# Optimization experiments

Measured on AMD Instinct MI355X. Metric: run time of the kernel, lower is better.

## Reference

```python
import jax, jax.numpy as jnp
import numpy as np

N, D, B, R, EF, K = 500000, 128, 512, 32, 64, 10
INF = 1e30  # sentinel distance for dead/duplicate slots


def setup_inputs() -> dict:
    key = jax.random.key(0)
    k1, k2, k3, k4 = jax.random.split(key, 4)
    return {
        "query": jax.random.normal(k1, (B, D), jnp.float32),
        "storage": jax.random.normal(k2, (N, D), jnp.float32),
        "indices": jax.random.randint(k3, (N, R), 0, N, dtype=jnp.int32),
        "entry": jax.random.randint(k4, (B, EF), 0, N, dtype=jnp.int32),
        "k": K,
        "ef_search": EF,
    }


def _merge(ids, dists, expanded, ef):
    # Dedup by node id (prefer the already-expanded copy so nodes are never
    # re-expanded), then keep the ef best candidates by distance.
    key = ids * 2 + (1 - expanded.astype(ids.dtype))  # expanded copy sorts first
    order = jnp.argsort(key)  # stable sort
    ids, dists, expanded = ids[order], dists[order], expanded[order]
    dup = jnp.concatenate([jnp.zeros((1,), bool), ids[1:] == ids[:-1]])
    dists = jnp.where(dup, INF, dists)       # kill duplicate slots
    expanded = jnp.where(dup, True, expanded)  # dead slots never selected
    order = jnp.argsort(dists)
    return ids[order][:ef], dists[order][:ef], expanded[order][:ef]


def _search_one(q, ep, storage, indices, ef):
    # Beam (priority-list) best-first NSW traversal for a single query,
    # ef steps of expand-best-unexpanded, batched-friendly formulation.
    d0 = jnp.sum((storage[ep] - q) ** 2, axis=-1)  # squared-L2 distances
    state = _merge(ep, d0, jnp.zeros(ep.shape, bool), ef)

    def step(carry, _):
        ids, dists, expanded = carry
        sel = jnp.argmin(jnp.where(expanded, INF, dists))  # best open node
        expanded = expanded.at[sel].set(True)
        nbrs = indices[ids[sel]]                           # [R] neighbor ids
        nd = jnp.sum((storage[nbrs] - q) ** 2, axis=-1)    # [R] distances
        carry = _merge(
            jnp.concatenate([ids, nbrs]),
            jnp.concatenate([dists, nd]),
            jnp.concatenate([expanded, jnp.zeros((R,), bool)]),
            ef,
        )
        return carry, None

    (ids, dists, _), _ = jax.lax.scan(step, state, None, length=ef)
    return ids, dists


def reference(query, storage, indices, entry, k, ef_search):
    ids, dists = jax.vmap(_search_one, in_axes=(0, 0, None, None, None))(
        query, entry, storage, indices, ef_search
    )
    return ids[:, :k], dists[:, :k]
```

## Files before the change

kernel.cpp:

```cpp
#include <hip/hip_runtime.h>
#include <stdint.h>

#define DIM 128
#define RNB 32
#define EFS 64
#define KTOP 10
#define INFD 1e30f

typedef unsigned long long u64;

__device__ __forceinline__ u64 shflx64(u64 v, int m) {
    return (u64)__shfl_xor((long long)v, m, 64);
}
__device__ __forceinline__ u64 dsperm64(int dst_byte, u64 v) {
    int lo = __builtin_amdgcn_ds_permute(dst_byte, (int)(unsigned)(v & 0xffffffffu));
    int hi = __builtin_amdgcn_ds_permute(dst_byte, (int)(unsigned)(v >> 32));
    return ((u64)(unsigned)hi << 32) | (unsigned)lo;
}
__device__ __forceinline__ u64 readlane64(u64 v, int l) {
    unsigned lo = (unsigned)__builtin_amdgcn_readlane((int)(unsigned)(v & 0xffffffffu), l);
    unsigned hi = (unsigned)__builtin_amdgcn_readlane((int)(unsigned)(v >> 32), l);
    return ((u64)hi << 32) | lo;
}
template <int CTRL>
__device__ __forceinline__ float dpp_add(float x) {
    int y = __builtin_amdgcn_mov_dpp(__float_as_int(x), CTRL, 0xF, 0xF, true);
    return x + __int_as_float(y);
}

__device__ __forceinline__ void bitonic128(u64 &e0, u64 &e1, int lane) {
    #pragma unroll
    for (int k = 2; k <= 128; k <<= 1) {
        #pragma unroll
        for (int j = k >> 1; j >= 1; j >>= 1) {
            if (j == 64) {
                u64 lo = e0 < e1 ? e0 : e1;
                u64 hi = e0 < e1 ? e1 : e0;
                e0 = lo; e1 = hi;
            } else {
                u64 o0 = shflx64(e0, j);
                u64 o1 = shflx64(e1, j);
                int i0 = lane, i1 = lane + 64;
                bool keepmin0 = ((i0 & k) == 0) == ((i0 & j) == 0);
                bool keepmin1 = ((i1 & k) == 0) == ((i1 & j) == 0);
                e0 = keepmin0 ? (e0 < o0 ? e0 : o0) : (e0 > o0 ? e0 : o0);
                e1 = keepmin1 ? (e1 < o1 ? e1 : o1) : (e1 > o1 ? e1 : o1);
            }
        }
    }
}

__device__ __forceinline__ void merge_slow(int n, int lane,
                                           int* ids_s, float* dst_s, int* exp_s,
                                           int* ids2, float* dst2, int* exp2) {
    __syncthreads();
    {
        int i1 = lane + 64;
        u64 e0 = ((u64)(uint32_t)(ids_s[lane] * 2 + (exp_s[lane] ? 0 : 1)) << 32) | (uint32_t)lane;
        u64 e1 = ~0ULL;
        if (i1 < n)
            e1 = ((u64)(uint32_t)(ids_s[i1] * 2 + (exp_s[i1] ? 0 : 1)) << 32) | (uint32_t)i1;
        bitonic128(e0, e1, lane);

        int id0 = -1, id1 = -1; float d0 = INFD, d1 = INFD; int x0 = 1, x1 = 1;
        { int p = (int)(e0 & 0xffffffffu); id0 = ids_s[p]; d0 = dst_s[p]; x0 = exp_s[p]; }
        if (e1 != ~0ULL) { int p = (int)(e1 & 0xffffffffu); id1 = ids_s[p]; d1 = dst_s[p]; x1 = exp_s[p]; }

        int prev0 = __shfl_up(id0, 1);
        int top0  = __shfl(id0, 63);
        int prev1 = __shfl_up(id1, 1);
        bool dup0 = (lane > 0) && (id0 == prev0);
        bool dup1 = (i1 < n) && (id1 == ((lane == 0) ? top0 : prev1));
        if (dup0) { d0 = INFD; x0 = 1; }
        if (dup1) { d1 = INFD; x1 = 1; }

        ids2[lane] = id0; dst2[lane] = d0; exp2[lane] = x0;
        ids2[i1]   = id1; dst2[i1]   = d1; exp2[i1]   = x1;

        u64 f0 = ((u64)__float_as_uint(d0) << 32) | (uint32_t)lane;
        u64 f1 = (i1 < n) ? (((u64)__float_as_uint(d1) << 32) | (uint32_t)i1) : ~0ULL;
        bitonic128(f0, f1, lane);

        int pf = (int)(f0 & 0xffffffffu);
        int idf = ids2[pf]; float df = dst2[pf]; int xf = exp2[pf];
        __syncthreads();
        ids_s[lane] = idf; dst_s[lane] = df; exp_s[lane] = xf;
    }
    __syncthreads();
}

#define LOAD_IDX(NODE) do {                                                    \
    size_t ib_ = (size_t)(NODE) * RNB;                                         \
    nid = indices[ib_ + (lane & 31)];                                          \
    int g0_ = lane >> 3;                                                       \
    ida = indices[ib_ + g0_];                                                  \
    idb = indices[ib_ + 8 + g0_];                                              \
    idc = indices[ib_ + 16 + g0_];                                             \
    idd = indices[ib_ + 24 + g0_];                                             \
} while (0)

#define LOAD_ROWS() do {                                                       \
    const float4* r0_ = (const float4*)(storage + (size_t)ida * DIM) + (lane & 7) * 4; \
    va[0][0] = r0_[0]; va[0][1] = r0_[1]; va[0][2] = r0_[2]; va[0][3] = r0_[3]; \
    const float4* r1_ = (const float4*)(storage + (size_t)idb * DIM) + (lane & 7) * 4; \
    va[1][0] = r1_[0]; va[1][1] = r1_[1]; va[1][2] = r1_[2]; va[1][3] = r1_[3]; \
    const float4* r2_ = (const float4*)(storage + (size_t)idc * DIM) + (lane & 7) * 4; \
    va[2][0] = r2_[0]; va[2][1] = r2_[1]; va[2][2] = r2_[2]; va[2][3] = r2_[3]; \
    const float4* r3_ = (const float4*)(storage + (size_t)idd * DIM) + (lane & 7) * 4; \
    va[3][0] = r3_[0]; va[3][1] = r3_[1]; va[3][2] = r3_[2]; va[3][3] = r3_[3]; \
} while (0)

#define POSTMERGE_STATE() do {                                                 \
    killmask = 0u;                                                             \
    _Pragma("unroll")                                                          \
    for (int j_ = 0; j_ < RNB; ++j_) {                                         \
        int idj_ = __builtin_amdgcn_readlane(nid, j_);                         \
        u64 beq_ = __ballot(bid == idj_);                                      \
        u64 neq_ = __ballot(nid == idj_);                                      \
        u64 kj_ = beq_ | (neq_ & ((1ull << j_) - 1ull));                       \
        killmask |= (kj_ ? 1u : 0u) << j_;                                     \
    }                                                                          \
    bkey = ((u64)__float_as_uint(bds) << 27)                                   \
         | ((u64)(unsigned)(bid * 2 + (bex ? 0 : 1)) << 7)                     \
         | (unsigned)lane;                                                     \
    bkey63 = readlane64(bkey, 63);                                             \
    u64 bo_ = __ballot(bex == 0);                                              \
    K_bopen = bo_ ? readlane64(bkey, (int)(__ffsll((long long)bo_) - 1)) : ~0ull; \
    use_slow = (__ballot(bds >= INFD) != 0ull);                                \
} while (0)

extern "C" __global__ __launch_bounds__(64, 1)
void nsw_search(const float* __restrict__ query,
                const float* __restrict__ storage,
                const int* __restrict__ indices,
                const int* __restrict__ entry,
                float* __restrict__ out,
                int B) {
    const int b = blockIdx.x;
    const int lane = threadIdx.x;

    __shared__ __align__(16) float q_s[DIM];
    __shared__ int   ids_s[96];
    __shared__ float dst_s[96];
    __shared__ int   exp_s[96];
    __shared__ int   ids2[128];
    __shared__ float dst2[128];
    __shared__ int   exp2[128];

    q_s[lane]      = query[(size_t)b * DIM + lane];
    q_s[64 + lane] = query[(size_t)b * DIM + 64 + lane];
    ids_s[lane] = entry[(size_t)b * EFS + lane];
    exp_s[lane] = 0;
    __syncthreads();

    {
        float4 ea[16];
        #pragma unroll
        for (int batch = 0; batch < 2; ++batch) {
            #pragma unroll
            for (int pp = 0; pp < 2; ++pp) {
                int p = batch * 2 + pp, g = p * 16 + (lane >> 2), sub = lane & 3;
                int id = ids_s[g];
                const float4* row = (const float4*)(storage + (size_t)id * DIM);
                #pragma unroll
                for (int c = 0; c < 8; ++c) ea[pp * 8 + c] = row[sub * 8 + c];
            }
            #pragma unroll
            for (int pp = 0; pp < 2; ++pp) {
                int p = batch * 2 + pp, g = p * 16 + (lane >> 2), sub = lane & 3;
                const float4* q4 = (const float4*)q_s;
                float acc = 0.f;
                #pragma unroll
                for (int c = 0; c < 8; ++c) {
                    float4 v = ea[pp * 8 + c];
                    float4 qv = q4[sub * 8 + c];
                    float dx = v.x - qv.x; acc = fmaf(dx, dx, acc);
                    dx = v.y - qv.y; acc = fmaf(dx, dx, acc);
                    dx = v.z - qv.z; acc = fmaf(dx, dx, acc);
                    dx = v.w - qv.w; acc = fmaf(dx, dx, acc);
                }
                acc += __shfl_xor(acc, 1);
                acc += __shfl_xor(acc, 2);
                if (sub == 0) dst_s[g] = acc;
            }
        }
    }

    merge_slow(64, lane, ids_s, dst_s, exp_s, ids2, dst2, exp2);

    int   bid = ids_s[lane];
    float bds = dst_s[lane];
    int   bex = exp_s[lane];

    float4 qv0, qv1, qv2, qv3;
    {
        const float4* q4 = (const float4*)q_s;
        int sub = lane & 7;
        qv0 = q4[sub * 4 + 0]; qv1 = q4[sub * 4 + 1];
        qv2 = q4[sub * 4 + 2]; qv3 = q4[sub * 4 + 3];
    }

    int nid, ida, idb, idc, idd;
    float4 va[4][4];
    unsigned killmask = 0;
    u64 K_bopen = ~0ull, bkey63 = ~0ull, bkey = 0;
    bool use_slow = false;

    {
        u64 open = __ballot(bex == 0);
        int sel = open ? (int)(__ffsll((long long)open) - 1) : 0;
        int node = __shfl(bid, sel);
        if (lane == sel) bex = 1;
        LOAD_IDX(node);
        LOAD_ROWS();
        POSTMERGE_STATE();
    }

    for (int step = 0; step < EFS; ++step) {
        const bool lastit = (step + 1 == EFS);

        float accs[4];
        #pragma unroll
        for (int p = 0; p < 4; ++p) {
            float acc = 0.f;
            float4 v;
            v = va[p][0];
            { float dx = v.x - qv0.x; acc = fmaf(dx, dx, acc);
              dx = v.y - qv0.y; acc = fmaf(dx, dx, acc);
              dx = v.z - qv0.z; acc = fmaf(dx, dx, acc);
              dx = v.w - qv0.w; acc = fmaf(dx, dx, acc); }
            v = va[p][1];
            { float dx = v.x - qv1.x; acc = fmaf(dx, dx, acc);
              dx = v.y - qv1.y; acc = fmaf(dx, dx, acc);
              dx = v.z - qv1.z; acc = fmaf(dx, dx, acc);
              dx = v.w - qv1.w; acc = fmaf(dx, dx, acc); }
            v = va[p][2];
            { float dx = v.x - qv2.x; acc = fmaf(dx, dx, acc);
              dx = v.y - qv2.y; acc = fmaf(dx, dx, acc);
              dx = v.z - qv2.z; acc = fmaf(dx, dx, acc);
              dx = v.w - qv2.w; acc = fmaf(dx, dx, acc); }
            v = va[p][3];
            { float dx = v.x - qv3.x; acc = fmaf(dx, dx, acc);
              dx = v.y - qv3.y; acc = fmaf(dx, dx, acc);
              dx = v.z - qv3.z; acc = fmaf(dx, dx, acc);
              dx = v.w - qv3.w; acc = fmaf(dx, dx, acc); }
            acc = dpp_add<0xB1>(acc);
            acc = dpp_add<0x4E>(acc);
            acc = dpp_add<0x104>(acc);
            accs[p] = acc;
        }
        int l8 = (lane & 7) << 3;
        float t0 = __shfl(accs[0], l8), t1 = __shfl(accs[1], l8);
        float t2 = __shfl(accs[2], l8), t3 = __shfl(accs[3], l8);
        int ps = (lane >> 3) & 3;
        float ndt = (ps & 2) ? ((ps & 1) ? t3 : t2) : ((ps & 1) ? t1 : t0);

        if (!use_slow) {
            bool kill = (killmask >> (lane & 31)) & 1u;
            float dk = kill ? INFD : ndt;
            u64 nkey = ((u64)__float_as_uint(dk) << 27)
                     | ((u64)(unsigned)(nid * 2 + 1) << 7)
                     | (unsigned)(64 + (lane & 31));

            u64 kmin = ~0ull; int rank = 0;
            #pragma unroll
            for (int j = 0; j < RNB; ++j) {
                u64 kj = readlane64(nkey, j);
                kmin = (kj < kmin) ? kj : kmin;
                rank += (kj < nkey) ? 1 : 0;
            }
            u64 K_minopen = (K_bopen < kmin) ? K_bopen : kmin;
            bool fallback = (K_minopen > bkey63);
            int node = fallback ? __builtin_amdgcn_readlane(bid, 0)
                                : (int)(((unsigned)((K_minopen >> 7) & 0xFFFFFu)) >> 1);

            if (!lastit) LOAD_IDX(node);

            u64 e1p = dsperm64((lane < 32) ? ((63 - rank) << 2) : 0, nkey);
            u64 e0 = bkey;
            u64 e1 = (lane < 32) ? ~0ull : e1p;
            { u64 lo = e0 < e1 ? e0 : e1; e0 = lo; }
            #pragma unroll
            for (int j = 32; j >= 1; j >>= 1) {
                u64 o0 = shflx64(e0, j);
                bool keepmin = (lane & j) == 0;
                e0 = keepmin ? (e0 < o0 ? e0 : o0) : (e0 > o0 ? e0 : o0);
            }
            bds = __uint_as_float((unsigned)(e0 >> 27));
            unsigned key1 = (unsigned)((e0 >> 7) & 0xFFFFFu);
            bid = (int)(key1 >> 1);
            bex = (int)((key1 & 1u) ^ 1u);
            if (!fallback && e0 == K_minopen) bex = 1;
        } else {
            ids_s[lane] = bid; dst_s[lane] = bds; exp_s[lane] = bex;
            if (lane < RNB) { ids_s[64 + lane] = nid; dst_s[64 + lane] = ndt; exp_s[64 + lane] = 0; }
            merge_slow(96, lane, ids_s, dst_s, exp_s, ids2, dst2, exp2);
            bid = ids_s[lane]; bds = dst_s[lane]; bex = exp_s[lane];
            u64 open = __ballot(bex == 0);
            int sel = open ? (int)(__ffsll((long long)open) - 1) : 0;
            int node = __shfl(bid, sel);
            if (lane == sel) bex = 1;
            if (!lastit) LOAD_IDX(node);
        }

        if (!lastit) {
            LOAD_ROWS();
            POSTMERGE_STATE();
        }
    }

    if (lane < KTOP) {
        out[(size_t)b * KTOP + lane] = (float)bid;
        out[(size_t)B * KTOP + (size_t)b * KTOP + lane] = bds;
    }
}

extern "C" void kernel_launch(void* const* d_in, const int* in_sizes, int n_in,
                              void* d_out, int out_size, void* d_ws, size_t ws_size,
                              hipStream_t stream) {
    const float* query   = (const float*)d_in[0];
    const float* storage = (const float*)d_in[1];
    const int*   indices = (const int*)d_in[2];
    const int*   entry   = (const int*)d_in[3];
    int B = in_sizes[0] / DIM;
    float* out = (float*)d_out;
    nsw_search<<<B, 64, 0, stream>>>(query, storage, indices, entry, out, B);
}
```

Before: 193.7 us.

## Prefetch neighbor lists of candidates to cut dependent index-load latency per step

Each step now preloads the adjacency rows of the 32 freshly loaded neighbors, plus the rows of the best open beam node and the fallback node. The next node's neighbor ids can then be picked from registers with bpermute instead of a dependent global load of the indices row, which removes one serialized memory round trip from the critical path of every step. The rank/min scan is also split into four independent chains to give more instruction-level parallelism. The cost is extra global loads and register pressure every step, with the slow merge path still using the old dependent load.

```diff
diff --git a/kernel.cpp b/kernel.cpp
--- a/kernel.cpp
+++ b/kernel.cpp
@@ -21,6 +21,12 @@
     unsigned lo = (unsigned)__builtin_amdgcn_readlane((int)(unsigned)(v & 0xffffffffu), l);
     unsigned hi = (unsigned)__builtin_amdgcn_readlane((int)(unsigned)(v >> 32), l);
     return ((u64)hi << 32) | lo;
+}
+__device__ __forceinline__ int bperm(int srclane, int v) {
+    return __builtin_amdgcn_ds_bpermute(srclane << 2, v);
+}
+__device__ __forceinline__ int4 sel4(bool c, int4 a, int4 b) {
+    return make_int4(c ? a.x : b.x, c ? a.y : b.y, c ? a.z : b.z, c ? a.w : b.w);
 }
 template <int CTRL>
 __device__ __forceinline__ float dpp_add(float x) {
@@ -110,6 +116,13 @@
     va[3][0] = r3_[0]; va[3][1] = r3_[1]; va[3][2] = r3_[2]; va[3][3] = r3_[3]; \
 } while (0)
 
+#define LOAD_NROW() do {                                                       \
+    nrow4[0] = *(const int4*)(indices + (size_t)ida * RNB + ((lane & 7) << 2)); \
+    nrow4[1] = *(const int4*)(indices + (size_t)idb * RNB + ((lane & 7) << 2)); \
+    nrow4[2] = *(const int4*)(indices + (size_t)idc * RNB + ((lane & 7) << 2)); \
+    nrow4[3] = *(const int4*)(indices + (size_t)idd * RNB + ((lane & 7) << 2)); \
+} while (0)
+
 #define POSTMERGE_STATE() do {                                                 \
     killmask = 0u;                                                             \
     _Pragma("unroll")                                                          \
@@ -127,6 +140,10 @@
     u64 bo_ = __ballot(bex == 0);                                              \
     K_bopen = bo_ ? readlane64(bkey, (int)(__ffsll((long long)bo_) - 1)) : ~0ull; \
     use_slow = (__ballot(bds >= INFD) != 0ull);                                \
+    int nb_ = bo_ ? (int)(((unsigned)((K_bopen >> 7) & 0xFFFFFu)) >> 1) : 0;   \
+    int nf_ = __builtin_amdgcn_readlane(bid, 0);                               \
+    pbeam = indices[(size_t)nb_ * RNB + (lane & 31)];                          \
+    pfall = indices[(size_t)nf_ * RNB + (lane & 31)];                          \
 } while (0)
 
 extern "C" __global__ __launch_bounds__(64, 1)
@@ -202,6 +219,8 @@
 
     int nid, ida, idb, idc, idd;
     float4 va[4][4];
+    int4 nrow4[4];
+    int pbeam = 0, pfall = 0;
     unsigned killmask = 0;
     u64 K_bopen = ~0ull, bkey63 = ~0ull, bkey = 0;
     bool use_slow = false;
@@ -213,6 +232,7 @@
         if (lane == sel) bex = 1;
         LOAD_IDX(node);
         LOAD_ROWS();
+        LOAD_NROW();
         POSTMERGE_STATE();
     }
 
@@ -262,19 +282,55 @@
                      | ((u64)(unsigned)(nid * 2 + 1) << 7)
                      | (unsigned)(64 + (lane & 31));
 
-            u64 kmin = ~0ull; int rank = 0;
+            u64 m0 = ~0ull, m1 = ~0ull, m2 = ~0ull, m3 = ~0ull;
+            int rank = 0;
             #pragma unroll
-            for (int j = 0; j < RNB; ++j) {
-                u64 kj = readlane64(nkey, j);
-                kmin = (kj < kmin) ? kj : kmin;
-                rank += (kj < nkey) ? 1 : 0;
-            }
+            for (int j = 0; j < 8; ++j) {
+                u64 k0 = readlane64(nkey, j);
+                u64 k1 = readlane64(nkey, 8 + j);
+                u64 k2 = readlane64(nkey, 16 + j);
+                u64 k3 = readlane64(nkey, 24 + j);
+                m0 = (k0 < m0) ? k0 : m0;
+                m1 = (k1 < m1) ? k1 : m1;
+                m2 = (k2 < m2) ? k2 : m2;
+                m3 = (k3 < m3) ? k3 : m3;
+                rank += (k0 < nkey) ? 1 : 0;
+                rank += (k1 < nkey) ? 1 : 0;
+                rank += (k2 < nkey) ? 1 : 0;
+                rank += (k3 < nkey) ? 1 : 0;
+            }
+            u64 ma = (m0 < m1) ? m0 : m1;
+            u64 mb = (m2 < m3) ? m2 : m3;
+            u64 kmin = (ma < mb) ? ma : mb;
+
             u64 K_minopen = (K_bopen < kmin) ? K_bopen : kmin;
             bool fallback = (K_minopen > bkey63);
-            int node = fallback ? __builtin_amdgcn_readlane(bid, 0)
-                                : (int)(((unsigned)((K_minopen >> 7) & 0xFFFFFu)) >> 1);
-
-            if (!lastit) LOAD_IDX(node);
+            bool win_new = !fallback && (kmin < K_bopen);
+            int w = (int)((unsigned)kmin & 127u) - 64;
+
+            int nid_n;
+            {
+                int kk = w >> 3;
+                int4 sA = sel4((kk & 2) != 0,
+                               sel4((kk & 1) != 0, nrow4[3], nrow4[2]),
+                               sel4((kk & 1) != 0, nrow4[1], nrow4[0]));
+                int src = ((w & 7) << 3) + ((lane & 31) >> 2);
+                int ex = bperm(src, sA.x);
+                int ey = bperm(src, sA.y);
+                int ez = bperm(src, sA.z);
+                int ew = bperm(src, sA.w);
+                int clo = (lane & 1) ? ey : ex;
+                int chi = (lane & 1) ? ew : ez;
+                int ext = (lane & 2) ? chi : clo;
+                int pb = fallback ? pfall : pbeam;
+                nid_n = win_new ? ext : pb;
+            }
+            ida = bperm(lane >> 3, nid_n);
+            idb = bperm(8 + (lane >> 3), nid_n);
+            idc = bperm(16 + (lane >> 3), nid_n);
+            idd = bperm(24 + (lane >> 3), nid_n);
+
+            if (!lastit) { LOAD_ROWS(); LOAD_NROW(); }
 
             u64 e1p = dsperm64((lane < 32) ? ((63 - rank) << 2) : 0, nkey);
             u64 e0 = bkey;
@@ -291,6 +347,8 @@
             bid = (int)(key1 >> 1);
             bex = (int)((key1 & 1u) ^ 1u);
             if (!fallback && e0 == K_minopen) bex = 1;
+
+            nid = nid_n;
         } else {
             ids_s[lane] = bid; dst_s[lane] = bds; exp_s[lane] = bex;
             if (lane < RNB) { ids_s[64 + lane] = nid; dst_s[64 + lane] = ndt; exp_s[64 + lane] = 0; }
@@ -300,13 +358,10 @@
             int sel = open ? (int)(__ffsll((long long)open) - 1) : 0;
             int node = __shfl(bid, sel);
             if (lane == sel) bex = 1;
-            if (!lastit) LOAD_IDX(node);
+            if (!lastit) { LOAD_IDX(node); LOAD_ROWS(); LOAD_NROW(); }
         }
 
-        if (!lastit) {
-            LOAD_ROWS();
-            POSTMERGE_STATE();
-        }
+        if (!lastit) POSTMERGE_STATE();
     }
 
     if (lane < KTOP) {
```

After: 211.4 us. 1.09x slower.
